# Performance work log

Hardware: AMD Instinct MI355X
Metric: run time of the kernel (lower is better)

## Reference

```python
import jax, jax.numpy as jnp
import numpy as np

N_ENT = 100000
N_REL = 500
D_IN = 128
D_OUT = 128
E_HALF = 1000000  # edges per direction; edge_index has 2*E_HALF columns
BN_EPS = 1e-5


def ccorr(a, b):
    # circular correlation: irfft(conj(rfft(a)) * rfft(b))
    d = a.shape[-1]
    return jnp.fft.irfft(jnp.conj(jnp.fft.rfft(a, axis=-1)) * jnp.fft.rfft(b, axis=-1), n=d, axis=-1)


def setup_inputs() -> dict:
    key = jax.random.key(0)
    ks = jax.random.split(key, 12)
    inv = 1.0 / np.sqrt(D_IN)
    inp = {
        "x": jax.random.normal(ks[0], (N_ENT, D_IN), dtype=jnp.float32),
        "rel_embed": jax.random.normal(ks[1], (N_REL, D_IN), dtype=jnp.float32),
        "w_in": jax.random.uniform(ks[2], (D_IN, D_OUT), minval=-inv, maxval=inv, dtype=jnp.float32),
        "w_out": jax.random.uniform(ks[3], (D_IN, D_OUT), minval=-inv, maxval=inv, dtype=jnp.float32),
        "w_loop": jax.random.uniform(ks[4], (D_IN, D_OUT), minval=-inv, maxval=inv, dtype=jnp.float32),
        "w_rel": jax.random.uniform(ks[5], (D_IN, D_OUT), minval=-inv, maxval=inv, dtype=jnp.float32),
        "loop_rel": jax.random.normal(ks[6], (1, D_IN), dtype=jnp.float32),
        "bias": jnp.zeros((D_OUT,), dtype=jnp.float32),
        "bn_weight": jnp.ones((D_OUT,), dtype=jnp.float32),
        "bn_bias": jnp.zeros((D_OUT,), dtype=jnp.float32),
        "edge_index": jax.random.randint(ks[7], (2, 2 * E_HALF), 0, N_ENT, dtype=jnp.int32),
        "edge_type": jax.random.randint(ks[8], (2 * E_HALF,), 0, N_REL, dtype=jnp.int32),
    }
    return inp


def _compute_norm(edge_index, num_ent):
    row, col = edge_index[0], edge_index[1]
    ones = jnp.ones(row.shape, dtype=jnp.float32)
    deg = jax.ops.segment_sum(ones, row, num_segments=num_ent)
    deg_inv = jnp.where(deg > 0, jax.lax.rsqrt(jnp.maximum(deg, 1.0)), 0.0)
    return deg_inv[row] * deg_inv[col]  # [E]


def _propagate(x, edge_index, edge_type, rel_all, weight, norm, num_ent):
    x_j = x[edge_index[0]]              # [E, d_in] gather source nodes
    r = rel_all[edge_type]              # [E, d_in] gather relation embeds
    m = ccorr(x_j, r) @ weight          # [E, d_out]
    if norm is not None:
        m = m * norm[:, None]
    return jax.ops.segment_sum(m, edge_index[1], num_segments=num_ent)


def reference(x, rel_embed, w_in, w_out, w_loop, w_rel, loop_rel, bias, bn_weight, bn_bias, edge_index, edge_type):
    num_ent = x.shape[0]
    rel_all = jnp.concatenate([rel_embed, loop_rel], axis=0)  # [R+1, d_in]
    e = edge_index.shape[1] // 2
    in_idx, out_idx = edge_index[:, :e], edge_index[:, e:]
    in_type, out_type = edge_type[:e], edge_type[e:]

    in_norm = _compute_norm(in_idx, num_ent)
    out_norm = _compute_norm(out_idx, num_ent)

    in_res = _propagate(x, in_idx, in_type, rel_all, w_in, in_norm, num_ent)
    out_res = _propagate(x, out_idx, out_type, rel_all, w_out, out_norm, num_ent)
    # loop edges are (i, i) with relation = last row of rel_all -> identity scatter
    loop_res = ccorr(x, rel_all[-1][None, :]) @ w_loop

    out = (in_res + out_res + loop_res) * (1.0 / 3.0) + bias
    # BatchNorm1d (training-mode batch statistics, biased variance)
    mu = jnp.mean(out, axis=0)
    var = jnp.mean((out - mu) ** 2, axis=0)
    out = (out - mu) * jax.lax.rsqrt(var + BN_EPS) * bn_weight + bn_bias

    rel_out = (rel_all @ w_rel)[:-1]
    return out, rel_out
```

## Files before the change

kernel.cpp:

```cpp
#include <hip/hip_runtime.h>
#include <cmath>

#define N_ENT 100000
#define EHALF 1000000
#define N_REL 500
#define NBUK 196
#define DPB 512
#define SCAP 7680
#define DCAP 6656

#ifndef M_PI
#define M_PI 3.14159265358979323846
#endif

typedef _Float16 f16x8 __attribute__((ext_vector_type(8)));
typedef _Float16 f16x4 __attribute__((ext_vector_type(4)));
typedef _Float16 f16x2 __attribute__((ext_vector_type(2)));
typedef float f32x4 __attribute__((ext_vector_type(4)));

union H16 { unsigned short u; _Float16 h; };
union HU32 { unsigned u; f16x2 h; };

__global__ void k_tabs(float* __restrict__ Ftab, float* __restrict__ Gtab,
                       _Float16* __restrict__ FtabT) {
  int i = blockIdx.x * 256 + threadIdx.x;
  if (i >= 128 * 128) return;
  int n = i >> 7, s = i & 127;
  float fv, gv;
  if (s == 0) { fv = 1.f; gv = 1.f / 384.f; }
  else if (s == 1) { float sg = (n & 1) ? -1.f : 1.f; fv = sg; gv = sg / 384.f; }
  else {
    int f = s >> 1;
    double ang = 2.0 * M_PI * (double)((f * n) & 127) / 128.0;
    if (!(s & 1)) { double c = cos(ang); fv = (float)c; gv = (float)(c * (2.0 / 384.0)); }
    else { double sv = sin(ang); fv = (float)(-sv); gv = (float)(-sv * (2.0 / 384.0)); }
  }
  Ftab[n * 128 + s] = fv;
  Gtab[s * 128 + n] = gv;
  FtabT[s * 128 + n] = (_Float16)fv;
}

__global__ void k_dftrel(const float* __restrict__ rel, const float* __restrict__ looprel,
                         const float* __restrict__ Ftab, float* __restrict__ Rf,
                         _Float16* __restrict__ RfL) {
  __shared__ float sv[128];
  int r = blockIdx.x, s = threadIdx.x;
  const float* row = (r < N_REL) ? rel + (size_t)r * 128 : looprel;
  float acc = 0.f;
  for (int n = 0; n < 128; ++n) acc += row[n] * Ftab[n * 128 + s];
  Rf[(size_t)r * 128 + s] = acc;
  sv[s] = acc;
  __syncthreads();
  if (s < 64) {
    f16x4 o;
    if (s == 0) {
      o = (f16x4){(_Float16)sv[0], (_Float16)0.f, (_Float16)0.f, (_Float16)sv[1]};
    } else {
      float rx = sv[2 * s], ry = sv[2 * s + 1];
      o = (f16x4){(_Float16)rx, (_Float16)ry, (_Float16)ry, (_Float16)(-rx)};
    }
    ((f16x4*)RfL)[(size_t)r * 64 + s] = o;
  }
}

__global__ void k_wt(const float* __restrict__ W, const float* __restrict__ Rfl,
                     _Float16* __restrict__ WT) {
  int i = blockIdx.x * 256 + threadIdx.x;
  if (i >= 384 * 128) return;
  int k = i >> 7, c = i & 127;
  float val;
  if (k < 256) {
    val = W[i];
  } else {
    int kk = k - 256;
    if (kk == 0)      val = Rfl[0] * W[i];
    else if (kk == 1) val = Rfl[1] * W[i];
    else {
      int f = kk >> 1;
      float rr = Rfl[2 * f], ri = Rfl[2 * f + 1];
      float a = W[(256 + 2 * f) * 128 + c];
      float b = W[(256 + 2 * f + 1) * 128 + c];
      val = (kk & 1) ? (ri * a - rr * b) : (rr * a + ri * b);
    }
  }
  WT[(size_t)c * 384 + k] = (_Float16)val;
}

__device__ void gemm128_body(const float* __restrict__ A, int lda,
                             const float* __restrict__ B,
                             float* __restrict__ C, int ldc,
                             int M, int K, int m0) {
  __shared__ float As[64][64];
  __shared__ float Bs[64][128];
  const int t = threadIdx.x;
  const int cg = t & 31;
  const int eg = t >> 5;
  float acc[8][4];
#pragma unroll
  for (int i = 0; i < 8; ++i)
#pragma unroll
    for (int j = 0; j < 4; ++j) acc[i][j] = 0.f;

  for (int k0 = 0; k0 < K; k0 += 64) {
#pragma unroll
    for (int p = 0; p < 4; ++p) {
      int idx = t + p * 256;
      int r = idx >> 4, c4 = idx & 15;
      int gr = m0 + r;
      float4 v = make_float4(0.f, 0.f, 0.f, 0.f);
      if (gr < M) v = *(const float4*)(A + (size_t)gr * lda + k0 + c4 * 4);
      *(float4*)&As[r][c4 * 4] = v;
    }
#pragma unroll
    for (int p = 0; p < 8; ++p) {
      int idx = t + p * 256;
      int r = idx >> 5, c4 = idx & 31;
      float4 v = *(const float4*)(B + (size_t)(k0 + r) * 128 + c4 * 4);
      *(float4*)&Bs[r][c4 * 4] = v;
    }
    __syncthreads();
#pragma unroll
    for (int k = 0; k < 64; ++k) {
      float4 bv = *(float4*)&Bs[k][cg * 4];
#pragma unroll
      for (int i = 0; i < 8; ++i) {
        float av = As[eg * 8 + i][k];
        acc[i][0] += av * bv.x; acc[i][1] += av * bv.y;
        acc[i][2] += av * bv.z; acc[i][3] += av * bv.w;
      }
    }
    __syncthreads();
  }
#pragma unroll
  for (int i = 0; i < 8; ++i) {
    int gr = m0 + eg * 8 + i;
    if (gr < M) {
      float4 v = make_float4(acc[i][0], acc[i][1], acc[i][2], acc[i][3]);
      *(float4*)(C + (size_t)gr * ldc + cg * 4) = v;
    }
  }
}

__global__ __launch_bounds__(256) void gemm128(
    const float* __restrict__ A, int lda, const float* __restrict__ B,
    float* __restrict__ C, int ldc, int M, int K) {
  gemm128_body(A, lda, B, C, ldc, M, K, blockIdx.x * 64);
}

__global__ __launch_bounds__(256) void k_wprep(
    const float* __restrict__ Gtab, const float* __restrict__ w0,
    const float* __restrict__ w1, const float* __restrict__ w2,
    float* __restrict__ Wstack) {
  int which = blockIdx.x >> 1;
  const float* B = (which == 0) ? w0 : ((which == 1) ? w1 : w2);
  gemm128_body(Gtab, 128, B, Wstack + which * 128 * 128, 128, 128, 128,
               (blockIdx.x & 1) * 64);
}

__device__ inline f16x8 loadAfrag(const _Float16* A, size_t off) {
  return *(const f16x8*)(A + off);
}
__device__ inline f16x8 loadAfrag(const float* A, size_t off) {
  float4 u = *(const float4*)(A + off);
  float4 v = *(const float4*)(A + off + 4);
  return (f16x8){(_Float16)u.x, (_Float16)u.y, (_Float16)u.z, (_Float16)u.w,
                 (_Float16)v.x, (_Float16)v.y, (_Float16)v.z, (_Float16)v.w};
}

template<int K, int KS, int MODE, typename AT>
__global__ __launch_bounds__(256) void mgemm(
    const AT* __restrict__ A, int lda,
    const _Float16* __restrict__ BT,
    _Float16* __restrict__ C, int ldc, int M,
    const float* __restrict__ bias, float* __restrict__ bnAcc) {
  __shared__ __align__(16) char lds[128 * KS * 2 + 4096];
  const int t = threadIdx.x;
  const int l = t & 63, w = t >> 6;
  const int col0 = l & 15, rg = l >> 4;
  const int rowbase = blockIdx.x * 256 + w * 64;
  const int sw = (col0 & 7) << 4;

  f32x4 acc[4][8];
  f32x4 zz = {0.f, 0.f, 0.f, 0.f};
#pragma unroll
  for (int a = 0; a < 4; ++a)
#pragma unroll
    for (int n = 0; n < 8; ++n) acc[a][n] = zz;

  for (int ks0 = 0; ks0 < K; ks0 += KS) {
    __syncthreads();
    const int CH = KS / 8;
    for (int u = t; u < 128 * CH; u += 256) {
      int col = u / CH, kc = u % CH;
      f16x8 vch = *(const f16x8*)(BT + (size_t)col * K + ks0 + kc * 8);
      *(f16x8*)(lds + col * (KS * 2) + ((kc * 16) ^ ((col & 7) << 4))) = vch;
    }
    __syncthreads();
#pragma unroll
    for (int ks = 0; ks < KS / 32; ++ks) {
      int kb = ks0 + ks * 32 + rg * 8;
      f16x8 af[4];
#pragma unroll
      for (int a = 0; a < 4; ++a) {
        int rb = rowbase + a * 16;
        if (rb < M) af[a] = loadAfrag(A, (size_t)(rb + col0) * lda + kb);
        else af[a] = (f16x8){0, 0, 0, 0, 0, 0, 0, 0};
      }
      int kc = ks * 4 + rg;
#pragma unroll
      for (int n = 0; n < 8; ++n) {
        f16x8 bf = *(const f16x8*)(lds + (n * 16 + col0) * (KS * 2) + ((kc * 16) ^ sw));
#pragma unroll
        for (int a = 0; a < 4; ++a)
          acc[a][n] = __builtin_amdgcn_mfma_f32_16x16x32_f16(af[a], bf, acc[a][n], 0, 0, 0);
      }
    }
  }

  if (MODE == 1) {
#pragma unroll
    for (int a = 0; a < 4; ++a) {
      int rb = rowbase + a * 16;
      if (rb >= M) continue;
#pragma unroll
      for (int r = 0; r < 4; ++r) {
        int row = rb + rg * 4 + r;
#pragma unroll
        for (int n = 0; n < 8; ++n) {
          int col = n * 16 + col0;
          C[(size_t)row * ldc + col] = (_Float16)acc[a][n][r];
        }
      }
    }
  } else {
    float sacc[8], qacc[8];
#pragma unroll
    for (int n = 0; n < 8; ++n) { sacc[n] = 0.f; qacc[n] = 0.f; }
#pragma unroll
    for (int a = 0; a < 4; ++a) {
      int rb = rowbase + a * 16;
      if (rb >= M) continue;
#pragma unroll
      for (int n = 0; n < 8; ++n) {
        int col = n * 16 + col0;
        float bi = bias[col];
#pragma unroll
        for (int r = 0; r < 4; ++r) {
          float val = acc[a][n][r] + bi;
          C[(size_t)(rb + rg * 4 + r) * ldc + col] = (_Float16)val;
          sacc[n] += val; qacc[n] += val * val;
        }
      }
    }
    __syncthreads();
    float* Sb = (float*)lds;
    float* Qb = Sb + 512;
#pragma unroll
    for (int n = 0; n < 8; ++n) {
      float s = sacc[n], q = qacc[n];
      s += __shfl_xor(s, 16); s += __shfl_xor(s, 32);
      q += __shfl_xor(q, 16); q += __shfl_xor(q, 32);
      if (rg == 0) { Sb[w * 128 + n * 16 + col0] = s; Qb[w * 128 + n * 16 + col0] = q; }
    }
    __syncthreads();
    if (t < 128) {
      float s = Sb[t] + Sb[128 + t] + Sb[256 + t] + Sb[384 + t];
      float q = Qb[t] + Qb[128 + t] + Qb[256 + t] + Qb[384 + t];
      atomicAdd(&bnAcc[t], s);
      atomicAdd(&bnAcc[128 + t], q);
    }
  }
}

__global__ __launch_bounds__(256) void k_splitS2(
    const int* __restrict__ ei,
    int* __restrict__ gSI, int* __restrict__ gSO,
    unsigned* __restrict__ recSI, unsigned* __restrict__ recSO) {
  __shared__ int bcnt[NBUK], cnt2[NBUK], base[NBUK], nn[NBUK];
  const int t = threadIdx.x;
  const int dir = blockIdx.x >> 8;
  const int blk = blockIdx.x & 255;
  const int* key = ei + (dir ? EHALF : 0);
  int* gcur = dir ? gSO : gSI;
  unsigned* rec = dir ? recSO : recSI;
  const int SPAN = 3907;
  int st = blk * SPAN;
  int en = min(st + SPAN, EHALF);
  if (t < NBUK) { bcnt[t] = 0; cnt2[t] = 0; }
  __syncthreads();
  unsigned rr[16]; int bb[16];
#pragma unroll
  for (int j = 0; j < 16; ++j) {
    int e = st + j * 256 + t;
    bb[j] = -1;
    if (e < en) {
      int s = key[e];
      rr[j] = (unsigned)(s & 511) | 0x80000000u;
      int b = s >> 9;
      bb[j] = b;
      atomicAdd(&bcnt[b], 1);
    }
  }
  __syncthreads();
  if (t < NBUK) {
    int n = bcnt[t]; nn[t] = n;
    base[t] = n ? (t * SCAP + atomicAdd(&gcur[t], (n + 7) & ~7)) : 0;
  }
  __syncthreads();
#pragma unroll
  for (int j = 0; j < 16; ++j) {
    if (bb[j] >= 0) {
      int p = atomicAdd(&cnt2[bb[j]], 1);
      rec[(size_t)base[bb[j]] + p] = rr[j];
    }
  }
  __syncthreads();
  if (t < NBUK) {
    int n = nn[t];
    if (n & 7) {
      int pe = (n + 7) & ~7;
      for (int k = n; k < pe; ++k) rec[(size_t)base[t] + k] = 0u;
    }
  }
}

__global__ __launch_bounds__(512) void k_dhist(
    const unsigned* __restrict__ recI, const int* __restrict__ gI,
    float* __restrict__ dinvIn,
    const unsigned* __restrict__ recO, const int* __restrict__ gO,
    float* __restrict__ dinvOut) {
  int b = blockIdx.x % NBUK;
  int dir = blockIdx.x / NBUK;
  const unsigned* rec = dir ? recO : recI;
  const int gs = b * SCAP;
  const int ge = gs + (dir ? gO : gI)[b];
  float* dinv = dir ? dinvOut : dinvIn;
  __shared__ int h[DPB];
  int t = threadIdx.x;
  h[t] = 0;
  __syncthreads();
  for (int i = gs + t; i < ge; i += 512) {
    unsigned r = rec[i];
    if (r >> 31) atomicAdd(&h[r & 511], 1);
  }
  __syncthreads();
  int ent = b * 512 + t;
  if (ent < N_ENT) {
    int d = h[t];
    dinv[ent] = (d > 0) ? rsqrtf((float)d) : 0.f;
  }
}

__global__ __launch_bounds__(256) void k_splitD2(
    const int* __restrict__ ei, const int* __restrict__ et,
    const float* __restrict__ dinvIn, const float* __restrict__ dinvOut,
    int* __restrict__ gDI, int* __restrict__ gDO,
    uint2* __restrict__ recDI, uint2* __restrict__ recDO) {
  __shared__ int bcnt[NBUK], cnt2[NBUK], base[NBUK], nn[NBUK];
  const int t = threadIdx.x;
  const int dir = blockIdx.x >> 8;
  const int blk = blockIdx.x & 255;
  const int* srcA = ei + (dir ? EHALF : 0);
  const int* dstA = ei + (dir ? 3 * EHALF : 2 * EHALF);
  const int* typA = et + (dir ? EHALF : 0);
  const float* dv = dir ? dinvOut : dinvIn;
  int* gcur = dir ? gDO : gDI;
  uint2* rec = dir ? recDO : recDI;
  const int SPAN = 3907;
  int st = blk * SPAN;
  int en = min(st + SPAN, EHALF);
  if (t < NBUK) { bcnt[t] = 0; cnt2[t] = 0; }
  __syncthreads();
  unsigned w0[16], w1[16]; int bb[16];
#pragma unroll
  for (int j = 0; j < 16; ++j) {
    int e = st + j * 256 + t;
    bb[j] = -1;
    if (e < en) {
      int s = srcA[e], d = dstA[e], ty = typA[e];
      float nm = dv[s] * dv[d];
      H16 cv; cv.h = (_Float16)nm;
      w0[j] = (unsigned)s | ((unsigned)ty << 17);
      w1[j] = (unsigned)(d & 511) | ((unsigned)cv.u << 16);
      int b = d >> 9;
      bb[j] = b;
      atomicAdd(&bcnt[b], 1);
    }
  }
  __syncthreads();
  if (t < NBUK) {
    int n = bcnt[t]; nn[t] = n;
    base[t] = n ? (t * DCAP + atomicAdd(&gcur[t], (n + 3) & ~3)) : 0;
  }
  __syncthreads();
#pragma unroll
  for (int j = 0; j < 16; ++j) {
    if (bb[j] >= 0) {
      int p = atomicAdd(&cnt2[bb[j]], 1);
      rec[(size_t)base[bb[j]] + p] = make_uint2(w0[j], w1[j]);
    }
  }
  __syncthreads();
  if (t < NBUK) {
    int n = nn[t];
    if (n & 3) {
      int pe = (n + 3) & ~3;
      for (int k = n; k < pe; ++k) rec[(size_t)base[t] + k] = make_uint2(0u, 0u);
    }
  }
}

__global__ __launch_bounds__(512) void k_fsort(
    const uint2* __restrict__ recDI, const int* __restrict__ gDI,
    uint2* __restrict__ csrIn, int2* __restrict__ beI,
    const uint2* __restrict__ recDO, const int* __restrict__ gDO,
    uint2* __restrict__ csrOut, int2* __restrict__ beO) {
  int b = blockIdx.x % NBUK;
  int dir = blockIdx.x / NBUK;
  const uint2* rec = dir ? recDO : recDI;
  const int gs = b * DCAP;
  const int ge = gs + (dir ? gDO : gDI)[b];
  uint2* csr = dir ? csrOut : csrIn;
  int2* be = dir ? beO : beI;
  __shared__ int h[DPB], sc[DPB], c2[DPB];
  int t = threadIdx.x;
  h[t] = 0; c2[t] = 0;
  __syncthreads();
  for (int i = gs + t; i < ge; i += 512) {
    uint2 r = rec[i];
    if (r.y >> 16) atomicAdd(&h[r.y & 511], 1);
  }
  __syncthreads();
  sc[t] = h[t];
  __syncthreads();
  for (int o = 1; o < 512; o <<= 1) {
    int a = (t >= o) ? sc[t - o] : 0;
    __syncthreads();
    sc[t] += a;
    __syncthreads();
  }
  int excl = sc[t] - h[t];
  int ent = b * 512 + t;
  if (ent < N_ENT) be[ent] = make_int2(gs + excl, gs + excl + h[t]);
  __syncthreads();
  sc[t] = excl;
  __syncthreads();
  for (int i = gs + t; i < ge; i += 512) {
    uint2 r = rec[i];
    if (r.y >> 16) {
      int d = r.y & 511;
      int p = atomicAdd(&c2[d], 1);
      csr[(size_t)gs + sc[d] + p] =
          make_uint2(((r.x & 0x1FFFFu) * 3u) << 8,
                     (r.x >> 17) | (r.y & 0xFFFF0000u));
    }
  }
}

__device__ inline float dot2f(f16x2 a, f16x2 b, float c) {
#if __has_builtin(__builtin_amdgcn_fdot2)
  return __builtin_amdgcn_fdot2(a, b, c, false);
#else
  return fmaf((float)a[0], (float)b[0], fmaf((float)a[1], (float)b[1], c));
#endif
}

__device__ inline void estep(uint2 q, const char* __restrict__ Xb,
                             const char* __restrict__ Rb,
                             unsigned lxc, unsigned lr, float& ax, float& ay) {
  f16x2 xv = *(const f16x2*)(Xb + q.x + lxc);
  f16x4 rv = *(const f16x4*)(Rb + ((q.y & 0x1FFu) << 9) + lr);
  HU32 nm; nm.u = (q.y >> 16) | (q.y & 0xFFFF0000u);
  f16x2 xs = xv * nm.h;
  f16x2 rlo = {rv[0], rv[1]}, rhi = {rv[2], rv[3]};
  ax = dot2f(xs, rlo, ax);
  ay = dot2f(xs, rhi, ay);
}

__global__ __launch_bounds__(256) void k_agg(
    _Float16* __restrict__ Abuf, const _Float16* __restrict__ RfL,
    const uint2* __restrict__ csrIn, const int2* __restrict__ beI,
    const uint2* __restrict__ csrOut, const int2* __restrict__ beO) {
  const int w = threadIdx.x >> 6, l = threadIdx.x & 63;
  const int v = blockIdx.x * 4 + w;
  const char* Xb = (const char*)Abuf;
  const char* Rb = (const char*)RfL;
  const unsigned lxc = 512u + (unsigned)l * 4u;
  const unsigned lr = (unsigned)l * 8u;
  int2 bi = beI[v], bo = beO[v];
  int i = bi.x, ie = bi.y;
  int o = bo.x, oe = bo.y;
  float aix = 0.f, aiy = 0.f, aox = 0.f, aoy = 0.f;

  while (i + 4 <= ie && o + 4 <= oe) {
    uint2 a0 = csrIn[i], a1 = csrIn[i + 1], a2 = csrIn[i + 2], a3 = csrIn[i + 3];
    uint2 b0 = csrOut[o], b1 = csrOut[o + 1], b2 = csrOut[o + 2], b3 = csrOut[o + 3];
    estep(a0, Xb, Rb, lxc, lr, aix, aiy);
    estep(b0, Xb, Rb, lxc, lr, aox, aoy);
    estep(a1, Xb, Rb, lxc, lr, aix, aiy);
    estep(b1, Xb, Rb, lxc, lr, aox, aoy);
    estep(a2, Xb, Rb, lxc, lr, aix, aiy);
    estep(b2, Xb, Rb, lxc, lr, aox, aoy);
    estep(a3, Xb, Rb, lxc, lr, aix, aiy);
    estep(b3, Xb, Rb, lxc, lr, aox, aoy);
    i += 4; o += 4;
  }
  while (i + 4 <= ie) {
    uint2 a0 = csrIn[i], a1 = csrIn[i + 1], a2 = csrIn[i + 2], a3 = csrIn[i + 3];
    estep(a0, Xb, Rb, lxc, lr, aix, aiy);
    estep(a1, Xb, Rb, lxc, lr, aix, aiy);
    estep(a2, Xb, Rb, lxc, lr, aix, aiy);
    estep(a3, Xb, Rb, lxc, lr, aix, aiy);
    i += 4;
  }
  while (o + 4 <= oe) {
    uint2 b0 = csrOut[o], b1 = csrOut[o + 1], b2 = csrOut[o + 2], b3 = csrOut[o + 3];
    estep(b0, Xb, Rb, lxc, lr, aox, aoy);
    estep(b1, Xb, Rb, lxc, lr, aox, aoy);
    estep(b2, Xb, Rb, lxc, lr, aox, aoy);
    estep(b3, Xb, Rb, lxc, lr, aox, aoy);
    o += 4;
  }
  while (i < ie) { estep(csrIn[i], Xb, Rb, lxc, lr, aix, aiy); ++i; }
  while (o < oe) { estep(csrOut[o], Xb, Rb, lxc, lr, aox, aoy); ++o; }

  *(f16x2*)((char*)Abuf + (size_t)v * 768 + 4u * l) = (f16x2){(_Float16)aix, (_Float16)aiy};
  *(f16x2*)((char*)Abuf + (size_t)v * 768 + 256 + 4u * l) = (f16x2){(_Float16)aox, (_Float16)aoy};
}

__global__ void k_bnfin(const float* __restrict__ bnAcc, const float* __restrict__ bnw,
                        const float* __restrict__ bnb, float* __restrict__ ss) {
  int c = threadIdx.x;
  float mu = bnAcc[c] * (1.f / (float)N_ENT);
  float var = bnAcc[128 + c] * (1.f / (float)N_ENT) - mu * mu;
  float sc = bnw[c] * rsqrtf(var + 1e-5f);
  ss[c] = sc; ss[128 + c] = bnb[c] - mu * sc;
}

__global__ void k_norm(const _Float16* __restrict__ tmp, float* __restrict__ out,
                       const float* __restrict__ ss) {
  int i = blockIdx.x * 256 + threadIdx.x;
  f16x8 v = ((const f16x8*)tmp)[i];
  int cb = (i & 15) * 8;
  float4 o0, o1;
  o0.x = (float)v[0] * ss[cb]     + ss[128 + cb];
  o0.y = (float)v[1] * ss[cb + 1] + ss[129 + cb];
  o0.z = (float)v[2] * ss[cb + 2] + ss[130 + cb];
  o0.w = (float)v[3] * ss[cb + 3] + ss[131 + cb];
  o1.x = (float)v[4] * ss[cb + 4] + ss[132 + cb];
  o1.y = (float)v[5] * ss[cb + 5] + ss[133 + cb];
  o1.z = (float)v[6] * ss[cb + 6] + ss[134 + cb];
  o1.w = (float)v[7] * ss[cb + 7] + ss[135 + cb];
  ((float4*)out)[2 * i] = o0;
  ((float4*)out)[2 * i + 1] = o1;
}

extern "C" void kernel_launch(void* const* d_in, const int* in_sizes, int n_in,
                              void* d_out, int out_size, void* d_ws, size_t ws_size,
                              hipStream_t stream) {
  const float* x       = (const float*)d_in[0];
  const float* rel     = (const float*)d_in[1];
  const float* w_in    = (const float*)d_in[2];
  const float* w_out   = (const float*)d_in[3];
  const float* w_loop  = (const float*)d_in[4];
  const float* w_rel   = (const float*)d_in[5];
  const float* looprel = (const float*)d_in[6];
  const float* bias    = (const float*)d_in[7];
  const float* bnw     = (const float*)d_in[8];
  const float* bnb     = (const float*)d_in[9];
  const int*   ei      = (const int*)d_in[10];
  const int*   et      = (const int*)d_in[11];
  float* out = (float*)d_out;

  char* p = (char*)d_ws;
  auto alloc = [&](size_t bytes) -> void* {
    void* r = (void*)p;
    p += (bytes + 255) & ~(size_t)255;
    return r;
  };
  _Float16* Abuf  = (_Float16*)alloc((size_t)N_ENT * 384 * 2);
  _Float16* tmpC  = (_Float16*)alloc((size_t)N_ENT * 128 * 2);
  _Float16* WT    = (_Float16*)alloc(128 * 384 * 2);
  _Float16* FtabT = (_Float16*)alloc(128 * 128 * 2);
  _Float16* RfL   = (_Float16*)alloc(501 * 64 * 4 * 2);
  float* Wstack   = (float*)alloc(384 * 128 * 4);
  float* Ftab     = (float*)alloc(128 * 128 * 4);
  float* Gtab     = (float*)alloc(128 * 128 * 4);
  float* Rf       = (float*)alloc(501 * 128 * 4);
  float* dinvIn   = (float*)alloc(N_ENT * 4);
  float* dinvOut  = (float*)alloc(N_ENT * 4);
  int*   gcur     = (int*)alloc(4 * NBUK * 4);
  int2*  beI      = (int2*)alloc((size_t)N_ENT * 8);
  int2*  beO      = (int2*)alloc((size_t)N_ENT * 8);
  unsigned* recSI = (unsigned*)alloc((size_t)NBUK * SCAP * 4);
  unsigned* recSO = (unsigned*)alloc((size_t)NBUK * SCAP * 4);
  uint2* recDI    = (uint2*)alloc((size_t)NBUK * DCAP * 8);
  uint2* recDO    = (uint2*)alloc((size_t)NBUK * DCAP * 8);
  uint2* csrIn    = (uint2*)alloc((size_t)NBUK * DCAP * 8);
  uint2* csrOut   = (uint2*)alloc((size_t)NBUK * DCAP * 8);
  float* bnAcc    = (float*)alloc(256 * 4);
  float* ss       = (float*)alloc(256 * 4);

  int* gSI = gcur;
  int* gSO = gcur + NBUK;
  int* gDI = gcur + 2 * NBUK;
  int* gDO = gcur + 3 * NBUK;

  hipMemsetAsync(gcur, 0, 4 * NBUK * 4, stream);
  hipMemsetAsync(bnAcc, 0, 256 * 4, stream);

  k_tabs<<<64, 256, 0, stream>>>(Ftab, Gtab, FtabT);
  k_dftrel<<<501, 128, 0, stream>>>(rel, looprel, Ftab, Rf, RfL);
  k_wprep<<<6, 256, 0, stream>>>(Gtab, w_in, w_out, w_loop, Wstack);
  k_wt<<<192, 256, 0, stream>>>(Wstack, Rf + 500 * 128, WT);

  mgemm<128, 128, 1, float><<<(N_ENT + 255) / 256, 256, 0, stream>>>(
      x, 128, FtabT, Abuf + 256, 384, N_ENT, nullptr, nullptr);

  k_splitS2<<<512, 256, 0, stream>>>(ei, gSI, gSO, recSI, recSO);
  k_dhist<<<2 * NBUK, 512, 0, stream>>>(recSI, gSI, dinvIn, recSO, gSO, dinvOut);
  k_splitD2<<<512, 256, 0, stream>>>(ei, et, dinvIn, dinvOut, gDI, gDO, recDI, recDO);
  k_fsort<<<2 * NBUK, 512, 0, stream>>>(recDI, gDI, csrIn, beI, recDO, gDO, csrOut, beO);

  k_agg<<<N_ENT / 4, 256, 0, stream>>>(Abuf, RfL, csrIn, beI, csrOut, beO);

  mgemm<384, 192, 2, _Float16><<<(N_ENT + 255) / 256, 256, 0, stream>>>(
      Abuf, 384, WT, tmpC, 128, N_ENT, bias, bnAcc);
  k_bnfin<<<1, 128, 0, stream>>>(bnAcc, bnw, bnb, ss);
  k_norm<<<(N_ENT * 128 / 8) / 256, 256, 0, stream>>>(tmpC, out, ss);

  gemm128<<<(N_REL + 63) / 64, 256, 0, stream>>>(rel, 128, w_rel, out + (size_t)N_ENT * 128, 128, N_REL, 128);
}
```

Baseline: 337.1 us.

## Fuse source and destination bucket splits, defer norm to fsort, batch agg loads

```diff
diff --git a/kernel.cpp b/kernel.cpp
--- a/kernel.cpp
+++ b/kernel.cpp
@@ -8,6 +8,8 @@
 #define DPB 512
 #define SCAP 7680
 #define DCAP 6656
+#define NSB 512
+#define SPAN 1954
 
 #ifndef M_PI
 #define M_PI 3.14159265358979323846
@@ -272,55 +274,101 @@
   }
 }
 
-__global__ __launch_bounds__(256) void k_splitS2(
-    const int* __restrict__ ei,
-    int* __restrict__ gSI, int* __restrict__ gSO,
-    unsigned* __restrict__ recSI, unsigned* __restrict__ recSO) {
+__global__ __launch_bounds__(256) void k_split(
+    const int* __restrict__ ei, const int* __restrict__ et,
+    int* __restrict__ gcur,
+    unsigned* __restrict__ recSI, unsigned* __restrict__ recSO,
+    uint2* __restrict__ recDI, uint2* __restrict__ recDO) {
   __shared__ int bcnt[NBUK], cnt2[NBUK], base[NBUK], nn[NBUK];
   const int t = threadIdx.x;
-  const int dir = blockIdx.x >> 8;
-  const int blk = blockIdx.x & 255;
-  const int* key = ei + (dir ? EHALF : 0);
-  int* gcur = dir ? gSO : gSI;
-  unsigned* rec = dir ? recSO : recSI;
-  const int SPAN = 3907;
-  int st = blk * SPAN;
-  int en = min(st + SPAN, EHALF);
-  if (t < NBUK) { bcnt[t] = 0; cnt2[t] = 0; }
-  __syncthreads();
-  unsigned rr[16]; int bb[16];
-#pragma unroll
-  for (int j = 0; j < 16; ++j) {
-    int e = st + j * 256 + t;
-    bb[j] = -1;
-    if (e < en) {
-      int s = key[e];
-      rr[j] = (unsigned)(s & 511) | 0x80000000u;
-      int b = s >> 9;
-      bb[j] = b;
-      atomicAdd(&bcnt[b], 1);
-    }
-  }
-  __syncthreads();
-  if (t < NBUK) {
-    int n = bcnt[t]; nn[t] = n;
-    base[t] = n ? (t * SCAP + atomicAdd(&gcur[t], (n + 7) & ~7)) : 0;
-  }
-  __syncthreads();
-#pragma unroll
-  for (int j = 0; j < 16; ++j) {
-    if (bb[j] >= 0) {
-      int p = atomicAdd(&cnt2[bb[j]], 1);
-      rec[(size_t)base[bb[j]] + p] = rr[j];
-    }
-  }
-  __syncthreads();
-  if (t < NBUK) {
-    int n = nn[t];
-    if (n & 7) {
-      int pe = (n + 7) & ~7;
-      for (int k = n; k < pe; ++k) rec[(size_t)base[t] + k] = 0u;
-    }
+  const int st = blockIdx.x * SPAN;
+  const int en = min(st + SPAN, EHALF);
+
+  for (int ph = 0; ph < 2; ++ph) {
+    const int* key = ei + (ph ? EHALF : 0);
+    int* gc = gcur + ph * NBUK;
+    unsigned* rec = ph ? recSO : recSI;
+    if (t < NBUK) { bcnt[t] = 0; cnt2[t] = 0; }
+    __syncthreads();
+    unsigned rr[8]; int bb[8];
+#pragma unroll
+    for (int j = 0; j < 8; ++j) {
+      int e = st + j * 256 + t;
+      bb[j] = -1;
+      if (e < en) {
+        int s = key[e];
+        rr[j] = (unsigned)(s & 511) | 0x80000000u;
+        bb[j] = s >> 9;
+        atomicAdd(&bcnt[bb[j]], 1);
+      }
+    }
+    __syncthreads();
+    if (t < NBUK) {
+      int n = bcnt[t]; nn[t] = n;
+      base[t] = n ? (t * SCAP + atomicAdd(&gc[t], (n + 7) & ~7)) : 0;
+    }
+    __syncthreads();
+#pragma unroll
+    for (int j = 0; j < 8; ++j) {
+      if (bb[j] >= 0) {
+        int p = atomicAdd(&cnt2[bb[j]], 1);
+        rec[(size_t)base[bb[j]] + p] = rr[j];
+      }
+    }
+    __syncthreads();
+    if (t < NBUK) {
+      int n = nn[t];
+      if (n & 7) {
+        int pe = (n + 7) & ~7;
+        for (int k = n; k < pe; ++k) rec[(size_t)base[t] + k] = 0u;
+      }
+    }
+    __syncthreads();
+  }
+
+  for (int ph = 0; ph < 2; ++ph) {
+    const int* srcA = ei + (ph ? EHALF : 0);
+    const int* dstA = ei + (ph ? 3 * EHALF : 2 * EHALF);
+    const int* typA = et + (ph ? EHALF : 0);
+    int* gc = gcur + (2 + ph) * NBUK;
+    uint2* rec = ph ? recDO : recDI;
+    if (t < NBUK) { bcnt[t] = 0; cnt2[t] = 0; }
+    __syncthreads();
+    unsigned w0[8], w1[8]; int bb[8];
+#pragma unroll
+    for (int j = 0; j < 8; ++j) {
+      int e = st + j * 256 + t;
+      bb[j] = -1;
+      if (e < en) {
+        int s = srcA[e], d = dstA[e], ty = typA[e];
+        w0[j] = (unsigned)s | ((unsigned)ty << 17);
+        w1[j] = (unsigned)(d & 511) | 0x80000000u;
+        bb[j] = d >> 9;
+        atomicAdd(&bcnt[bb[j]], 1);
+      }
+    }
+    __syncthreads();
+    if (t < NBUK) {
+      int n = bcnt[t]; nn[t] = n;
+      base[t] = n ? (t * DCAP + atomicAdd(&gc[t], (n + 3) & ~3)) : 0;
+    }
+    __syncthreads();
+#pragma unroll
+    for (int j = 0; j < 8; ++j) {
+      if (bb[j] >= 0) {
+        int p = atomicAdd(&cnt2[bb[j]], 1);
+        rec[(size_t)base[bb[j]] + p] = make_uint2(w0[j], w1[j]);
+      }
+    }
+    __syncthreads();
+    if (t < NBUK) {
+      int n = nn[t];
+      if (n & 3) {
+        int pe = (n + 3) & ~3;
+        for (int k = n; k < pe; ++k) rec[(size_t)base[t] + k] = make_uint2(0u, 0u);
+      }
+    }
+    __syncthreads();
   }
 }
 
@@ -351,84 +399,31 @@
   }
 }
 
-__global__ __launch_bounds__(256) void k_splitD2(
-    const int* __restrict__ ei, const int* __restrict__ et,
-    const float* __restrict__ dinvIn, const float* __restrict__ dinvOut,
-    int* __restrict__ gDI, int* __restrict__ gDO,
-    uint2* __restrict__ recDI, uint2* __restrict__ recDO) {
-  __shared__ int bcnt[NBUK], cnt2[NBUK], base[NBUK], nn[NBUK];
-  const int t = threadIdx.x;
-  const int dir = blockIdx.x >> 8;
-  const int blk = blockIdx.x & 255;
-  const int* srcA = ei + (dir ? EHALF : 0);
-  const int* dstA = ei + (dir ? 3 * EHALF : 2 * EHALF);
-  const int* typA = et + (dir ? EHALF : 0);
-  const float* dv = dir ? dinvOut : dinvIn;
-  int* gcur = dir ? gDO : gDI;
-  uint2* rec = dir ? recDO : recDI;
-  const int SPAN = 3907;
-  int st = blk * SPAN;
-  int en = min(st + SPAN, EHALF);
-  if (t < NBUK) { bcnt[t] = 0; cnt2[t] = 0; }
-  __syncthreads();
-  unsigned w0[16], w1[16]; int bb[16];
-#pragma unroll
-  for (int j = 0; j < 16; ++j) {
-    int e = st + j * 256 + t;
-    bb[j] = -1;
-    if (e < en) {
-      int s = srcA[e], d = dstA[e], ty = typA[e];
-      float nm = dv[s] * dv[d];
-      H16 cv; cv.h = (_Float16)nm;
-      w0[j] = (unsigned)s | ((unsigned)ty << 17);
-      w1[j] = (unsigned)(d & 511) | ((unsigned)cv.u << 16);
-      int b = d >> 9;
-      bb[j] = b;
-      atomicAdd(&bcnt[b], 1);
-    }
-  }
-  __syncthreads();
-  if (t < NBUK) {
-    int n = bcnt[t]; nn[t] = n;
-    base[t] = n ? (t * DCAP + atomicAdd(&gcur[t], (n + 3) & ~3)) : 0;
-  }
-  __syncthreads();
-#pragma unroll
-  for (int j = 0; j < 16; ++j) {
-    if (bb[j] >= 0) {
-      int p = atomicAdd(&cnt2[bb[j]], 1);
-      rec[(size_t)base[bb[j]] + p] = make_uint2(w0[j], w1[j]);
-    }
-  }
-  __syncthreads();
-  if (t < NBUK) {
-    int n = nn[t];
-    if (n & 3) {
-      int pe = (n + 3) & ~3;
-      for (int k = n; k < pe; ++k) rec[(size_t)base[t] + k] = make_uint2(0u, 0u);
-    }
-  }
-}
-
 __global__ __launch_bounds__(512) void k_fsort(
     const uint2* __restrict__ recDI, const int* __restrict__ gDI,
     uint2* __restrict__ csrIn, int2* __restrict__ beI,
     const uint2* __restrict__ recDO, const int* __restrict__ gDO,
-    uint2* __restrict__ csrOut, int2* __restrict__ beO) {
+    uint2* __restrict__ csrOut, int2* __restrict__ beO,
+    const float* __restrict__ dinvIn, const float* __restrict__ dinvOut) {
   int b = blockIdx.x % NBUK;
   int dir = blockIdx.x / NBUK;
   const uint2* rec = dir ? recDO : recDI;
   const int gs = b * DCAP;
   const int ge = gs + (dir ? gDO : gDI)[b];
+  const float* dinv = dir ? dinvOut : dinvIn;
   uint2* csr = dir ? csrOut : csrIn;
   int2* be = dir ? beO : beI;
   __shared__ int h[DPB], sc[DPB], c2[DPB];
+  __shared__ float dl[DPB];
+  __shared__ int totv;
   int t = threadIdx.x;
+  int ent = b * 512 + t;
   h[t] = 0; c2[t] = 0;
+  dl[t] = (ent < N_ENT) ? dinv[ent] : 0.f;
   __syncthreads();
   for (int i = gs + t; i < ge; i += 512) {
     uint2 r = rec[i];
-    if (r.y >> 16) atomicAdd(&h[r.y & 511], 1);
+    if (r.y >> 31) atomicAdd(&h[r.y & 511], 1);
   }
   __syncthreads();
   sc[t] = h[t];
@@ -440,19 +435,23 @@
     __syncthreads();
   }
   int excl = sc[t] - h[t];
-  int ent = b * 512 + t;
+  if (t == 511) totv = sc[511];
   if (ent < N_ENT) be[ent] = make_int2(gs + excl, gs + excl + h[t]);
   __syncthreads();
   sc[t] = excl;
   __syncthreads();
+  if (t < 8) csr[(size_t)gs + totv + t] = make_uint2(0u, 0u);
   for (int i = gs + t; i < ge; i += 512) {
     uint2 r = rec[i];
-    if (r.y >> 16) {
+    if (r.y >> 31) {
       int d = r.y & 511;
+      unsigned src = r.x & 0x1FFFFu;
+      float nm = dinv[src] * dl[d];
+      H16 cv; cv.h = (_Float16)nm;
       int p = atomicAdd(&c2[d], 1);
       csr[(size_t)gs + sc[d] + p] =
-          make_uint2(((r.x & 0x1FFFFu) * 3u) << 8,
-                     (r.x >> 17) | (r.y & 0xFFFF0000u));
+          make_uint2((src * 3u) << 8,
+                     (r.x >> 17) | ((unsigned)cv.u << 16));
     }
   }
 }
@@ -465,16 +464,29 @@
 #endif
 }
 
-__device__ inline void estep(uint2 q, const char* __restrict__ Xb,
-                             const char* __restrict__ Rb,
-                             unsigned lxc, unsigned lr, float& ax, float& ay) {
-  f16x2 xv = *(const f16x2*)(Xb + q.x + lxc);
-  f16x4 rv = *(const f16x4*)(Rb + ((q.y & 0x1FFu) << 9) + lr);
-  HU32 nm; nm.u = (q.y >> 16) | (q.y & 0xFFFF0000u);
-  f16x2 xs = xv * nm.h;
-  f16x2 rlo = {rv[0], rv[1]}, rhi = {rv[2], rv[3]};
-  ax = dot2f(xs, rlo, ax);
-  ay = dot2f(xs, rhi, ay);
+__device__ inline void b4load(const uint2* __restrict__ csr, int base,
+                              const char* __restrict__ Xb, const char* __restrict__ Rb,
+                              unsigned lxc, unsigned lr,
+                              uint2 q[4], f16x2 xv[4], f16x4 rv[4]) {
+#pragma unroll
+  for (int j = 0; j < 4; ++j) q[j] = csr[base + j];
+#pragma unroll
+  for (int j = 0; j < 4; ++j) {
+    xv[j] = *(const f16x2*)(Xb + q[j].x + lxc);
+    rv[j] = *(const f16x4*)(Rb + ((q[j].y & 0x1FFu) << 9) + lr);
+  }
+}
+__device__ inline void b4math(const uint2 q[4], int base, int end,
+                              const f16x2 xv[4], const f16x4 rv[4],
+                              float& ax, float& ay) {
+#pragma unroll
+  for (int j = 0; j < 4; ++j) {
+    unsigned nb = (base + j < end) ? (q[j].y >> 16) : 0u;
+    HU32 nm; nm.u = nb | (nb << 16);
+    f16x2 xs = xv[j] * nm.h;
+    ax = dot2f(xs, (f16x2){rv[j][0], rv[j][1]}, ax);
+    ay = dot2f(xs, (f16x2){rv[j][2], rv[j][3]}, ay);
+  }
 }
 
 __global__ __launch_bounds__(256) void k_agg(
@@ -488,41 +500,34 @@
   const unsigned lxc = 512u + (unsigned)l * 4u;
   const unsigned lr = (unsigned)l * 8u;
   int2 bi = beI[v], bo = beO[v];
-  int i = bi.x, ie = bi.y;
-  int o = bo.x, oe = bo.y;
+  int i  = __builtin_amdgcn_readfirstlane(bi.x);
+  int ie = __builtin_amdgcn_readfirstlane(bi.y);
+  int o  = __builtin_amdgcn_readfirstlane(bo.x);
+  int oe = __builtin_amdgcn_readfirstlane(bo.y);
+  int nbi = (ie - i + 3) >> 2;
+  int nbo = (oe - o + 3) >> 2;
   float aix = 0.f, aiy = 0.f, aox = 0.f, aoy = 0.f;
 
-  while (i + 4 <= ie && o + 4 <= oe) {
-    uint2 a0 = csrIn[i], a1 = csrIn[i + 1], a2 = csrIn[i + 2], a3 = csrIn[i + 3];
-    uint2 b0 = csrOut[o], b1 = csrOut[o + 1], b2 = csrOut[o + 2], b3 = csrOut[o + 3];
-    estep(a0, Xb, Rb, lxc, lr, aix, aiy);
-    estep(b0, Xb, Rb, lxc, lr, aox, aoy);
-    estep(a1, Xb, Rb, lxc, lr, aix, aiy);
-    estep(b1, Xb, Rb, lxc, lr, aox, aoy);
-    estep(a2, Xb, Rb, lxc, lr, aix, aiy);
-    estep(b2, Xb, Rb, lxc, lr, aox, aoy);
-    estep(a3, Xb, Rb, lxc, lr, aix, aiy);
-    estep(b3, Xb, Rb, lxc, lr, aox, aoy);
-    i += 4; o += 4;
-  }
-  while (i + 4 <= ie) {
-    uint2 a0 = csrIn[i], a1 = csrIn[i + 1], a2 = csrIn[i + 2], a3 = csrIn[i + 3];
-    estep(a0, Xb, Rb, lxc, lr, aix, aiy);
-    estep(a1, Xb, Rb, lxc, lr, aix, aiy);
-    estep(a2, Xb, Rb, lxc, lr, aix, aiy);
-    estep(a3, Xb, Rb, lxc, lr, aix, aiy);
-    i += 4;
-  }
-  while (o + 4 <= oe) {
-    uint2 b0 = csrOut[o], b1 = csrOut[o + 1], b2 = csrOut[o + 2], b3 = csrOut[o + 3];
-    estep(b0, Xb, Rb, lxc, lr, aox, aoy);
-    estep(b1, Xb, Rb, lxc, lr, aox, aoy);
-    estep(b2, Xb, Rb, lxc, lr, aox, aoy);
-    estep(b3, Xb, Rb, lxc, lr, aox, aoy);
-    o += 4;
-  }
-  while (i < ie) { estep(csrIn[i], Xb, Rb, lxc, lr, aix, aiy); ++i; }
-  while (o < oe) { estep(csrOut[o], Xb, Rb, lxc, lr, aox, aoy); ++o; }
+  while (nbi > 0 && nbo > 0) {
+    uint2 qa[4], qb[4]; f16x2 xa[4], xb[4]; f16x4 ra[4], rb[4];
+    b4load(csrIn, i, Xb, Rb, lxc, lr, qa, xa, ra);
+    b4load(csrOut, o, Xb, Rb, lxc, lr, qb, xb, rb);
+    b4math(qa, i, ie, xa, ra, aix, aiy);
+    b4math(qb, o, oe, xb, rb, aox, aoy);
+    i += 4; o += 4; --nbi; --nbo;
+  }
+  while (nbi > 0) {
+    uint2 qa[4]; f16x2 xa[4]; f16x4 ra[4];
+    b4load(csrIn, i, Xb, Rb, lxc, lr, qa, xa, ra);
+    b4math(qa, i, ie, xa, ra, aix, aiy);
+    i += 4; --nbi;
+  }
+  while (nbo > 0) {
+    uint2 qb[4]; f16x2 xb[4]; f16x4 rb[4];
+    b4load(csrOut, o, Xb, Rb, lxc, lr, qb, xb, rb);
+    b4math(qb, o, oe, xb, rb, aox, aoy);
+    o += 4; --nbo;
+  }
 
   *(f16x2*)((char*)Abuf + (size_t)v * 768 + 4u * l) = (f16x2){(_Float16)aix, (_Float16)aiy};
   *(f16x2*)((char*)Abuf + (size_t)v * 768 + 256 + 4u * l) = (f16x2){(_Float16)aox, (_Float16)aoy};
@@ -617,10 +622,10 @@
   mgemm<128, 128, 1, float><<<(N_ENT + 255) / 256, 256, 0, stream>>>(
       x, 128, FtabT, Abuf + 256, 384, N_ENT, nullptr, nullptr);
 
-  k_splitS2<<<512, 256, 0, stream>>>(ei, gSI, gSO, recSI, recSO);
+  k_split<<<NSB, 256, 0, stream>>>(ei, et, gcur, recSI, recSO, recDI, recDO);
   k_dhist<<<2 * NBUK, 512, 0, stream>>>(recSI, gSI, dinvIn, recSO, gSO, dinvOut);
-  k_splitD2<<<512, 256, 0, stream>>>(ei, et, dinvIn, dinvOut, gDI, gDO, recDI, recDO);
-  k_fsort<<<2 * NBUK, 512, 0, stream>>>(recDI, gDI, csrIn, beI, recDO, gDO, csrOut, beO);
+  k_fsort<<<2 * NBUK, 512, 0, stream>>>(recDI, gDI, csrIn, beI, recDO, gDO, csrOut, beO,
+                                        dinvIn, dinvOut);
 
   k_agg<<<N_ENT / 4, 256, 0, stream>>>(Abuf, RfL, csrIn, beI, csrOut, beO);
 
```

Result: faster. 324.9 us (-3.6%).
